# Optimization experiments

Measured on AMD Instinct MI355X. Metric: run time of the kernel, lower is better.

## Reference

```python
import jax, jax.numpy as jnp
import numpy as np

NUM_HEADS = 8
EPS = 1e-12  # torch F.normalize eps

def _conv(x, w, padding, groups=1):
    return jax.lax.conv_general_dilated(
        x, w, window_strides=(1, 1), padding=padding,
        dimension_numbers=('NCHW', 'OIHW', 'NCHW'),
        feature_group_count=groups)

def setup_inputs() -> dict:
    key = jax.random.key(0)
    ks = jax.random.split(key, 5)
    b, dim, h, w = 8, 192, 128, 128
    kv = jax.random.normal(ks[0], (b, dim, h, w), dtype=jnp.float32)
    q = jax.random.normal(ks[1], (b, dim, h, w), dtype=jnp.float32)
    qkv1_w = jax.random.normal(ks[2], (2 * dim, dim, 1, 1), dtype=jnp.float32) * (1.0 / np.sqrt(dim))
    qkv2_w = jax.random.normal(ks[3], (2 * dim, 1, 3, 3), dtype=jnp.float32) * (1.0 / 3.0)
    proj_w = jax.random.normal(ks[4], (dim, dim, 1, 1), dtype=jnp.float32) * (1.0 / np.sqrt(dim))
    scale = jnp.ones((NUM_HEADS, 1, 1), dtype=jnp.float32)
    return {"kv": kv, "q": q, "qkv1_w": qkv1_w, "qkv2_w": qkv2_w,
            "proj_w": proj_w, "scale": scale}

def reference(kv, q, qkv1_w, qkv2_w, proj_w, scale):
    b, c, h, w = kv.shape
    head = NUM_HEADS
    cd = c // head  # channels per head
    hw = h * w
    # 1x1 conv dim -> 2*dim, then 3x3 depthwise conv (groups = 2*dim)
    kv_f = _conv(kv, qkv1_w, padding='VALID')
    kv_f = _conv(kv_f, qkv2_w, padding=((1, 1), (1, 1)), groups=2 * c)
    k, v = jnp.split(kv_f, 2, axis=1)
    # rearrange to [b, head, c, hw]
    qh = q.reshape(b, head, cd, hw)
    kh = k.reshape(b, head, cd, hw)
    vh = v.reshape(b, head, cd, hw)
    # L2-normalize along spatial dim (torch F.normalize semantics)
    qh = qh / jnp.maximum(jnp.linalg.norm(qh, axis=-1, keepdims=True), EPS)
    kh = kh / jnp.maximum(jnp.linalg.norm(kh, axis=-1, keepdims=True), EPS)
    # channel attention: [b, head, c, c]
    attn = jnp.einsum('bhcn,bhdn->bhcd', qh, kh) * scale  # scale broadcasts [head,1,1]
    attn = jax.nn.softmax(attn, axis=-1)
    out = jnp.einsum('bhcd,bhdn->bhcn', attn, vh)  # [b, head, c, hw]
    out = out.reshape(b, c, h, w)
    out = _conv(out, proj_w, padding='VALID')
    return out
```

## Files before the change

### kernel.cpp

```cpp
#include <hip/hip_runtime.h>
#include <hip/hip_bf16.h>

#define HW 16384
#define DIM 192
#define DIM2 384
#define NB 8
#define HEADS 8
#define CD 24
#define NSPLIT 64

typedef float f32x4 __attribute__((ext_vector_type(4)));
typedef short bf16x8 __attribute__((ext_vector_type(8)));
typedef short s16x4 __attribute__((ext_vector_type(4)));

__device__ __forceinline__ short f2bf(float f) {
    __hip_bfloat16 h = __float2bfloat16(f);
    return *reinterpret_cast<short*>(&h);
}
__device__ __forceinline__ float bf2f(short s) {
    __hip_bfloat16 h = *reinterpret_cast<__hip_bfloat16*>(&s);
    return __bfloat162float(h);
}

__global__ __launch_bounds__(256)
void prep_w1(const float* __restrict__ w1, short* __restrict__ wb1)
{
    int idx = blockIdx.x * 256 + threadIdx.x;
    if (idx >= 9216) return;
    int mi = idx / 384, rem = idx % 384;
    int c = rem >> 6, l = rem & 63;
    int oc = mi * 16 + (l & 15);
    int kb = c * 32 + (l >> 4) * 8;
    const float* src = w1 + (long)oc * DIM + kb;
    float4 v0 = *reinterpret_cast<const float4*>(src);
    float4 v1 = *reinterpret_cast<const float4*>(src + 4);
    bf16x8 o;
    o[0]=f2bf(v0.x); o[1]=f2bf(v0.y); o[2]=f2bf(v0.z); o[3]=f2bf(v0.w);
    o[4]=f2bf(v1.x); o[5]=f2bf(v1.y); o[6]=f2bf(v1.z); o[7]=f2bf(v1.w);
    *reinterpret_cast<bf16x8*>(wb1 + (long)idx * 8) = o;
}

template<int NOCT, bool B_F32, bool PER_BATCH_A, bool OUT_F32>
__global__ __launch_bounds__(256, 2)
void gemm_k192(const short* __restrict__ Ab, const void* __restrict__ Bg,
               void* __restrict__ Cg, long bstrideB, long bstrideC)
{
    __shared__ short lds[128 * 200];
    __shared__ float eps[4][16 * 36];
    const int tid  = threadIdx.x;
    const int lane = tid & 63;
    const int wave = tid >> 6;
    const int pxbase = blockIdx.x * 256;
    const int b    = blockIdx.y;

    const int row  = lane & 15;
    const int kgrp = lane >> 4;
    const short* A0 = Ab + (PER_BATCH_A ? (long)b * NOCT * 3072 : 0);

    bf16x8 aA[6], aB[6];
    auto loadA = [&](bf16x8* dst, int mi) {
#pragma unroll
        for (int c = 0; c < 6; c++)
            dst[c] = *reinterpret_cast<const bf16x8*>(
                &A0[((long)(mi * 6 + c) * 64 + lane) * 8]);
    };

    const int q  = tid & 31;
    const int kl = tid >> 5;
    f32x4 stf[6][4];
    s16x4 sth[6][4];
    auto SLOADJ = [&](int px0, int j) {
        if constexpr (B_F32) {
            const float* src = (const float*)Bg + (long)b * bstrideB + px0 + q * 4;
#pragma unroll
            for (int e = 0; e < 4; e++)
                stf[j][e] = __builtin_nontemporal_load(
                    reinterpret_cast<const f32x4*>(src + (long)(32 * j + 4 * kl + e) * HW));
        } else {
            const short* src = (const short*)Bg + (long)b * bstrideB + px0 + q * 4;
#pragma unroll
            for (int e = 0; e < 4; e++)
                sth[j][e] = __builtin_nontemporal_load(
                    reinterpret_cast<const s16x4*>(src + (long)(32 * j + 4 * kl + e) * HW));
        }
    };
    auto SWRITEJ = [&](int j) {
        const int goff = (((kl >> 1) ^ (q & 3)) << 3) + (kl & 1) * 4;
#pragma unroll
        for (int i = 0; i < 4; i++) {
            s16x4 t;
            if constexpr (B_F32)
                t = (s16x4){f2bf(stf[j][0][i]), f2bf(stf[j][1][i]),
                            f2bf(stf[j][2][i]), f2bf(stf[j][3][i])};
            else
                t = (s16x4){sth[j][0][i], sth[j][1][i], sth[j][2][i], sth[j][3][i]};
            *(s16x4*)&lds[(q * 4 + i) * 200 + 32 * j + goff] = t;
        }
    };

    bf16x8 bv[2][6];
    auto HOIST = [&]() {
        const int bro = wave * 32 + row;
        const int sgr = (row >> 2) & 3;
#pragma unroll
        for (int c = 0; c < 6; c++) {
            bv[0][c] = *(const bf16x8*)&lds[bro * 200 + c * 32 + ((kgrp ^ sgr) << 3)];
            bv[1][c] = *(const bf16x8*)&lds[(bro + 16) * 200 + c * 32 + ((kgrp ^ sgr) << 3)];
        }
    };

    const int ocl = lane >> 2;
    float* ep = &eps[wave][0];
    auto computeStore = [&](const bf16x8* a, int mi, int px0) {
        f32x4 acc0 = (f32x4){0.f, 0.f, 0.f, 0.f};
        f32x4 acc1 = (f32x4){0.f, 0.f, 0.f, 0.f};
#pragma unroll
        for (int c = 0; c < 6; c++) {
            acc0 = __builtin_amdgcn_mfma_f32_16x16x32_bf16(a[c], bv[0][c], acc0, 0, 0, 0);
            acc1 = __builtin_amdgcn_mfma_f32_16x16x32_bf16(a[c], bv[1][c], acc1, 0, 0, 0);
        }
#pragma unroll
        for (int r = 0; r < 4; r++) {
            ep[(kgrp * 4 + r) * 36 + row]      = acc0[r];
            ep[(kgrp * 4 + r) * 36 + 16 + row] = acc1[r];
        }
#pragma unroll
        for (int t = 0; t < 2; t++) {
            const int pxq = (lane & 3) + t * 4;
            f32x4 vv = *reinterpret_cast<const f32x4*>(&ep[ocl * 36 + pxq * 4]);
            long off = (long)b * bstrideC + (long)(mi * 16 + ocl) * HW
                     + px0 + wave * 32 + pxq * 4;
            if constexpr (OUT_F32) {
                __builtin_nontemporal_store(vv, reinterpret_cast<f32x4*>((float*)Cg + off));
            } else {
                *reinterpret_cast<s16x4*>((short*)Cg + off) =
                    (s16x4){f2bf(vv[0]), f2bf(vv[1]), f2bf(vv[2]), f2bf(vv[3])};
            }
        }
    };

    loadA(aA, 0);
    SLOADJ(pxbase, 0); SLOADJ(pxbase, 1); SLOADJ(pxbase, 2);
    SWRITEJ(0); SLOADJ(pxbase, 3);
    SWRITEJ(1); SLOADJ(pxbase, 4);
    SWRITEJ(2); SLOADJ(pxbase, 5);
    SWRITEJ(3); SWRITEJ(4); SWRITEJ(5);
    __syncthreads();
    HOIST();
    __syncthreads();

    SLOADJ(pxbase + 128, 0); SLOADJ(pxbase + 128, 1); SLOADJ(pxbase + 128, 2);
#pragma unroll
    for (int mi = 0; mi < NOCT; mi += 2) {
        loadA(aB, mi + 1);
        computeStore(aA, mi, pxbase);
        if (mi + 2 < NOCT) loadA(aA, mi + 2);
        const int p = mi >> 1;
        if (p < 3) SLOADJ(pxbase + 128, p + 3);
        if (p < 6) SWRITEJ(p);
        computeStore(aB, mi + 1, pxbase);
    }
    loadA(aA, 0);
    __syncthreads();
    HOIST();

#pragma unroll
    for (int mi = 0; mi < NOCT; mi += 2) {
        loadA(aB, mi + 1);
        computeStore(aA, mi, pxbase + 128);
        if (mi + 2 < NOCT) loadA(aA, mi + 2);
        computeStore(aB, mi + 1, pxbase + 128);
    }
}

__global__ __launch_bounds__(256)
void dwconv_sumsq(const short* __restrict__ in, const float* __restrict__ w2,
                  short* __restrict__ outp, float* __restrict__ kss)
{
    __shared__ float red[4];
    const long bgc = blockIdx.x;
    const int  gc  = (int)(bgc % DIM2);
    const int  b   = (int)(bgc / DIM2);
    const int  tid = threadIdx.x;
    const int  tx  = tid & 15;
    const int  ty  = tid >> 4;
    const int  lane = tid & 63;
    const int  x0 = tx * 8;
    const int  y0 = ty * 8;
    const short* src = in + (bgc << 14);
    short* dst = outp + (bgc << 14);

    float w[9];
#pragma unroll
    for (int i = 0; i < 9; i++) w[i] = w2[gc * 9 + i];

    float r0[10], r1[10], r2[10];
    auto loadRow = [&](float* r, int y) {
        if ((unsigned)y > 127u) {
#pragma unroll
            for (int i = 0; i < 10; i++) r[i] = 0.f;
            return;
        }
        bf16x8 v = *reinterpret_cast<const bf16x8*>(&src[y * 128 + x0]);
#pragma unroll
        for (int i = 0; i < 8; i++) r[i + 1] = bf2f(v[i]);
        float left  = __shfl(r[8], lane - 1);
        float right = __shfl(r[1], lane + 1);
        r[0] = (tx == 0)  ? 0.f : left;
        r[9] = (tx == 15) ? 0.f : right;
    };

    loadRow(r0, y0 - 1);
    loadRow(r1, y0);
    float ssq = 0.f;
#pragma unroll
    for (int k = 0; k < 8; k++) {
        const int yy = y0 + k;
        loadRow(r2, yy + 1);
        bf16x8 o;
#pragma unroll
        for (int j = 0; j < 8; j++) {
            float s = r0[j] * w[0] + r0[j + 1] * w[1] + r0[j + 2] * w[2]
                    + r1[j] * w[3] + r1[j + 1] * w[4] + r1[j + 2] * w[5]
                    + r2[j] * w[6] + r2[j + 1] * w[7] + r2[j + 2] * w[8];
            o[j] = f2bf(s);
            ssq += s * s;
        }
        *reinterpret_cast<bf16x8*>(&dst[yy * 128 + x0]) = o;
#pragma unroll
        for (int i = 0; i < 10; i++) { r0[i] = r1[i]; r1[i] = r2[i]; }
    }

    for (int o = 32; o; o >>= 1) ssq += __shfl_xor(ssq, o);
    if ((tid & 63) == 0) red[tid >> 6] = ssq;
    __syncthreads();
    if (gc < DIM && tid == 0)
        kss[b * DIM + gc] = red[0] + red[1] + red[2] + red[3];
}

__global__ __launch_bounds__(64)
void qk_mfma(const float* __restrict__ q, const short* __restrict__ kvb,
             float* __restrict__ part, float* __restrict__ pssq)
{
    const int split = blockIdx.x;
    const int bh    = blockIdx.y;
    const int b = bh >> 3, h = bh & 7;
    const int lane = threadIdx.x;
    const int row = lane & 15;
    const int kg  = (lane >> 4) * 8;
    const int CHUNK = HW / NSPLIT;

    const int qr1 = min(h * CD + 16 + row, DIM - 1);
    const float* q0 = q + ((long)b * DIM + h * CD + row) * HW + split * CHUNK + kg;
    const float* q1 = q + ((long)b * DIM + qr1) * HW + split * CHUNK + kg;
    const short* k0 = kvb + ((long)b * DIM2 + h * CD + row) * HW + split * CHUNK + kg;
    const short* k1 = k0 + 16L * HW;

    f32x4 acc[2][2];
#pragma unroll
    for (int m = 0; m < 2; m++)
#pragma unroll
        for (int n = 0; n < 2; n++) acc[m][n] = (f32x4){0.f, 0.f, 0.f, 0.f};
    float ssq0 = 0.f, ssq1 = 0.f;

#pragma unroll
    for (int s = 0; s < CHUNK / 32; s++) {
        const int px = s * 32;
        float4 qa = *reinterpret_cast<const float4*>(q0 + px);
        float4 qb = *reinterpret_cast<const float4*>(q0 + px + 4);
        float4 qc = *reinterpret_cast<const float4*>(q1 + px);
        float4 qd = *reinterpret_cast<const float4*>(q1 + px + 4);
        bf16x8 b0 = *reinterpret_cast<const bf16x8*>(k0 + px);
        bf16x8 b1 = *reinterpret_cast<const bf16x8*>(k1 + px);
        ssq0 += qa.x*qa.x + qa.y*qa.y + qa.z*qa.z + qa.w*qa.w
              + qb.x*qb.x + qb.y*qb.y + qb.z*qb.z + qb.w*qb.w;
        ssq1 += qc.x*qc.x + qc.y*qc.y + qc.z*qc.z + qc.w*qc.w
              + qd.x*qd.x + qd.y*qd.y + qd.z*qd.z + qd.w*qd.w;
        bf16x8 a0, a1;
        a0[0]=f2bf(qa.x); a0[1]=f2bf(qa.y); a0[2]=f2bf(qa.z); a0[3]=f2bf(qa.w);
        a0[4]=f2bf(qb.x); a0[5]=f2bf(qb.y); a0[6]=f2bf(qb.z); a0[7]=f2bf(qb.w);
        a1[0]=f2bf(qc.x); a1[1]=f2bf(qc.y); a1[2]=f2bf(qc.z); a1[3]=f2bf(qc.w);
        a1[4]=f2bf(qd.x); a1[5]=f2bf(qd.y); a1[6]=f2bf(qd.z); a1[7]=f2bf(qd.w);
        acc[0][0] = __builtin_amdgcn_mfma_f32_16x16x32_bf16(a0, b0, acc[0][0], 0, 0, 0);
        acc[0][1] = __builtin_amdgcn_mfma_f32_16x16x32_bf16(a0, b1, acc[0][1], 0, 0, 0);
        acc[1][0] = __builtin_amdgcn_mfma_f32_16x16x32_bf16(a1, b0, acc[1][0], 0, 0, 0);
        acc[1][1] = __builtin_amdgcn_mfma_f32_16x16x32_bf16(a1, b1, acc[1][1], 0, 0, 0);
    }

    ssq0 += __shfl_xor(ssq0, 16); ssq0 += __shfl_xor(ssq0, 32);
    ssq1 += __shfl_xor(ssq1, 16); ssq1 += __shfl_xor(ssq1, 32);

    float* pd = part + ((long)split * 64 + bh) * 576;
#pragma unroll
    for (int m = 0; m < 2; m++)
#pragma unroll
        for (int n = 0; n < 2; n++)
#pragma unroll
            for (int r = 0; r < 4; r++) {
                int c = m * 16 + (lane >> 4) * 4 + r;
                int d = n * 16 + row;
                if (c < CD && d < CD) pd[c * CD + d] = acc[m][n][r];
            }
    if (lane < 16) {
        float* ps = pssq + ((long)split * 64 + bh) * 32;
        ps[lane]      = ssq0;
        ps[16 + lane] = ssq1;
    }
}

__global__ __launch_bounds__(64)
void softmax_kernel(const float* __restrict__ part, const float* __restrict__ pssq,
                    const float* __restrict__ kss, const float* __restrict__ scale,
                    float* __restrict__ prob)
{
    const int blk = blockIdx.x;
    const int b = blk / DIM;
    const int hc = blk % DIM;
    const int h = hc / CD, c = hc % CD;
    const int bh = b * 8 + h;
    const int d = threadIdx.x;

    float qs = 0.f;
    for (int s = 0; s < NSPLIT; s++) qs += pssq[((long)s * 64 + bh) * 32 + c];

    float val = -1e30f;
    if (d < CD) {
        float raw = 0.f;
        for (int s = 0; s < NSPLIT; s++) raw += part[((long)s * 64 + bh) * 576 + c * CD + d];
        float qn = fmaxf(sqrtf(qs), 1e-12f);
        float kn = fmaxf(sqrtf(kss[b * DIM + h * CD + d]), 1e-12f);
        val = raw * scale[h] / (qn * kn);
    }
    float m = val;
    for (int o = 32; o; o >>= 1) m = fmaxf(m, __shfl_xor(m, o));
    float e = (d < CD) ? expf(val - m) : 0.f;
    float s = e;
    for (int o = 32; o; o >>= 1) s += __shfl_xor(s, o);
    if (d < CD) prob[(long)blk * CD + d] = e / s;
}

__global__ __launch_bounds__(256)
void buildm(const float* __restrict__ pw, const float* __restrict__ prob,
            short* __restrict__ M)
{
    int idx = blockIdx.x * 256 + threadIdx.x;
    if (idx >= 36864) return;
    int b   = idx / 4608, rem = idx % 4608;
    int mi  = rem / 384, r2 = rem % 384;
    int c   = r2 >> 6, l = r2 & 63;
    int oc  = mi * 16 + (l & 15);
    int gb  = c * 32 + (l >> 4) * 8;
    bf16x8 o;
#pragma unroll
    for (int e = 0; e < 8; e++) {
        int gvc = gb + e;
        int h = gvc / CD, d = gvc % CD;
        float s = 0.f;
#pragma unroll
        for (int cc = 0; cc < CD; cc++)
            s += pw[oc * DIM + h * CD + cc] * prob[((long)b * DIM + h * CD + cc) * CD + d];
        o[e] = f2bf(s);
    }
    *reinterpret_cast<bf16x8*>(M + (long)idx * 8) = o;
}

extern "C" void kernel_launch(void* const* d_in, const int* in_sizes, int n_in,
                              void* d_out, int out_size, void* d_ws, size_t ws_size,
                              hipStream_t stream)
{
    const float* kv    = (const float*)d_in[0];
    const float* q     = (const float*)d_in[1];
    const float* w1    = (const float*)d_in[2];
    const float* w2    = (const float*)d_in[3];
    const float* pw    = (const float*)d_in[4];
    const float* scale = (const float*)d_in[5];
    float* out = (float*)d_out;

    char* ws = (char*)d_ws;
    long off = 0;
    auto alloc = [&](long bytes) { char* p = ws + off; off += (bytes + 255) & ~255L; return p; };
    short* kvf1 = (short*)alloc((long)NB * DIM2 * HW * 2);
    short* kvb  = (short*)alloc((long)NB * DIM2 * HW * 2);
    short* wb1  = (short*)alloc((long)DIM2 * DIM * 2);
    float* kss  = (float*)alloc((long)NB * DIM * 4);
    float* part = (float*)alloc((long)NSPLIT * 64 * 576 * 4);
    float* pssq = (float*)alloc((long)NSPLIT * 64 * 32 * 4);
    float* prob = (float*)alloc((long)64 * 576 * 4);
    short* M    = (short*)alloc((long)NB * DIM * DIM * 2);

    prep_w1<<<36, 256, 0, stream>>>(w1, wb1);

    gemm_k192<24, true, false, false><<<dim3(64, NB), 256, 0, stream>>>(
        wb1, kv, kvf1, (long)DIM * HW, (long)DIM2 * HW);

    dwconv_sumsq<<<NB * DIM2, 256, 0, stream>>>(kvf1, w2, kvb, kss);

    qk_mfma<<<dim3(NSPLIT, 64), 64, 0, stream>>>(q, kvb, part, pssq);

    softmax_kernel<<<NB * DIM, 64, 0, stream>>>(part, pssq, kss, scale, prob);

    buildm<<<144, 256, 0, stream>>>(pw, prob, M);

    gemm_k192<12, false, true, true><<<dim3(64, NB), 256, 0, stream>>>(
        M, kvb + (long)DIM * HW, out, (long)DIM2 * HW, (long)DIM * HW);
}
```

Before: 201.2 us.

## Shrink GEMM blocks to single-wave 32-pixel tiles with more blocks

```diff
diff --git a/kernel.cpp b/kernel.cpp
--- a/kernel.cpp
+++ b/kernel.cpp
@@ -41,16 +41,13 @@
 }
 
 template<int NOCT, bool B_F32, bool PER_BATCH_A, bool OUT_F32>
-__global__ __launch_bounds__(256, 2)
+__global__ __launch_bounds__(64, 3)
 void gemm_k192(const short* __restrict__ Ab, const void* __restrict__ Bg,
                void* __restrict__ Cg, long bstrideB, long bstrideC)
 {
-    __shared__ short lds[128 * 200];
-    __shared__ float eps[4][16 * 36];
-    const int tid  = threadIdx.x;
-    const int lane = tid & 63;
-    const int wave = tid >> 6;
-    const int pxbase = blockIdx.x * 256;
+    __shared__ short lds[32 * 200];
+    const int lane = threadIdx.x;
+    const int px0  = blockIdx.x * 32;
     const int b    = blockIdx.y;
 
     const int row  = lane & 15;
@@ -65,19 +62,19 @@
                 &A0[((long)(mi * 6 + c) * 64 + lane) * 8]);
     };
 
-    const int q  = tid & 31;
-    const int kl = tid >> 5;
+    const int q2 = lane & 7;
+    const int kl = lane >> 3;
     f32x4 stf[6][4];
     s16x4 sth[6][4];
-    auto SLOADJ = [&](int px0, int j) {
+    auto SLOADJ = [&](int j) {
         if constexpr (B_F32) {
-            const float* src = (const float*)Bg + (long)b * bstrideB + px0 + q * 4;
+            const float* src = (const float*)Bg + (long)b * bstrideB + px0 + q2 * 4;
 #pragma unroll
             for (int e = 0; e < 4; e++)
                 stf[j][e] = __builtin_nontemporal_load(
                     reinterpret_cast<const f32x4*>(src + (long)(32 * j + 4 * kl + e) * HW));
         } else {
-            const short* src = (const short*)Bg + (long)b * bstrideB + px0 + q * 4;
+            const short* src = (const short*)Bg + (long)b * bstrideB + px0 + q2 * 4;
 #pragma unroll
             for (int e = 0; e < 4; e++)
                 sth[j][e] = __builtin_nontemporal_load(
@@ -85,7 +82,7 @@
         }
     };
     auto SWRITEJ = [&](int j) {
-        const int goff = (((kl >> 1) ^ (q & 3)) << 3) + (kl & 1) * 4;
+        const int goff = (((kl >> 1) ^ (q2 & 3)) << 3) + (kl & 1) * 4;
 #pragma unroll
         for (int i = 0; i < 4; i++) {
             s16x4 t;
@@ -94,24 +91,31 @@
                             f2bf(stf[j][2][i]), f2bf(stf[j][3][i])};
             else
                 t = (s16x4){sth[j][0][i], sth[j][1][i], sth[j][2][i], sth[j][3][i]};
-            *(s16x4*)&lds[(q * 4 + i) * 200 + 32 * j + goff] = t;
-        }
-    };
+            *(s16x4*)&lds[(q2 * 4 + i) * 200 + 32 * j + goff] = t;
+        }
+    };
+
+    loadA(aA, 0);
+    SLOADJ(0); SLOADJ(1); SLOADJ(2);
+    SWRITEJ(0); SLOADJ(3);
+    SWRITEJ(1); SLOADJ(4);
+    SWRITEJ(2); SLOADJ(5);
+    SWRITEJ(3); SWRITEJ(4); SWRITEJ(5);
 
     bf16x8 bv[2][6];
-    auto HOIST = [&]() {
-        const int bro = wave * 32 + row;
+    {
         const int sgr = (row >> 2) & 3;
 #pragma unroll
         for (int c = 0; c < 6; c++) {
-            bv[0][c] = *(const bf16x8*)&lds[bro * 200 + c * 32 + ((kgrp ^ sgr) << 3)];
-            bv[1][c] = *(const bf16x8*)&lds[(bro + 16) * 200 + c * 32 + ((kgrp ^ sgr) << 3)];
-        }
-    };
+            bv[0][c] = *(const bf16x8*)&lds[row * 200 + c * 32 + ((kgrp ^ sgr) << 3)];
+            bv[1][c] = *(const bf16x8*)&lds[(row + 16) * 200 + c * 32 + ((kgrp ^ sgr) << 3)];
+        }
+    }
+
+    float* ep = reinterpret_cast<float*>(&lds[0]);
 
     const int ocl = lane >> 2;
-    float* ep = &eps[wave][0];
-    auto computeStore = [&](const bf16x8* a, int mi, int px0) {
+    auto computeStore = [&](const bf16x8* a, int mi) {
         f32x4 acc0 = (f32x4){0.f, 0.f, 0.f, 0.f};
         f32x4 acc1 = (f32x4){0.f, 0.f, 0.f, 0.f};
 #pragma unroll
@@ -129,7 +133,7 @@
             const int pxq = (lane & 3) + t * 4;
             f32x4 vv = *reinterpret_cast<const f32x4*>(&ep[ocl * 36 + pxq * 4]);
             long off = (long)b * bstrideC + (long)(mi * 16 + ocl) * HW
-                     + px0 + wave * 32 + pxq * 4;
+                     + px0 + pxq * 4;
             if constexpr (OUT_F32) {
                 __builtin_nontemporal_store(vv, reinterpret_cast<f32x4*>((float*)Cg + off));
             } else {
@@ -139,37 +143,12 @@
         }
     };
 
-    loadA(aA, 0);
-    SLOADJ(pxbase, 0); SLOADJ(pxbase, 1); SLOADJ(pxbase, 2);
-    SWRITEJ(0); SLOADJ(pxbase, 3);
-    SWRITEJ(1); SLOADJ(pxbase, 4);
-    SWRITEJ(2); SLOADJ(pxbase, 5);
-    SWRITEJ(3); SWRITEJ(4); SWRITEJ(5);
-    __syncthreads();
-    HOIST();
-    __syncthreads();
-
-    SLOADJ(pxbase + 128, 0); SLOADJ(pxbase + 128, 1); SLOADJ(pxbase + 128, 2);
 #pragma unroll
     for (int mi = 0; mi < NOCT; mi += 2) {
         loadA(aB, mi + 1);
-        computeStore(aA, mi, pxbase);
+        computeStore(aA, mi);
         if (mi + 2 < NOCT) loadA(aA, mi + 2);
-        const int p = mi >> 1;
-        if (p < 3) SLOADJ(pxbase + 128, p + 3);
-        if (p < 6) SWRITEJ(p);
-        computeStore(aB, mi + 1, pxbase);
-    }
-    loadA(aA, 0);
-    __syncthreads();
-    HOIST();
-
-#pragma unroll
-    for (int mi = 0; mi < NOCT; mi += 2) {
-        loadA(aB, mi + 1);
-        computeStore(aA, mi, pxbase + 128);
-        if (mi + 2 < NOCT) loadA(aA, mi + 2);
-        computeStore(aB, mi + 1, pxbase + 128);
+        computeStore(aB, mi + 1);
     }
 }
 
@@ -390,7 +369,7 @@
 
     prep_w1<<<36, 256, 0, stream>>>(w1, wb1);
 
-    gemm_k192<24, true, false, false><<<dim3(64, NB), 256, 0, stream>>>(
+    gemm_k192<24, true, false, false><<<dim3(512, NB), 64, 0, stream>>>(
         wb1, kv, kvf1, (long)DIM * HW, (long)DIM2 * HW);
 
     dwconv_sumsq<<<NB * DIM2, 256, 0, stream>>>(kvf1, w2, kvb, kss);
@@ -401,6 +380,6 @@
 
     buildm<<<144, 256, 0, stream>>>(pw, prob, M);
 
-    gemm_k192<12, false, true, true><<<dim3(64, NB), 256, 0, stream>>>(
+    gemm_k192<12, false, true, true><<<dim3(512, NB), 64, 0, stream>>>(
         M, kvb + (long)DIM * HW, out, (long)DIM2 * HW, (long)DIM * HW);
 }
```

Result: slower. 217.4 us (+8.1%).
